# Kernel optimization log

Hardware: AMD Instinct MI355X
Metric: run time of the kernel (lower is better)

The kernel has to match this reference:

```python
import jax, jax.numpy as jnp
import numpy as np

B, NPG, FDIM = 128, 32, 128      # graphs, nodes per graph, feature dim
N = B * NPG                       # 4096 total nodes
DEG = 8
E = N * DEG                       # 32768 intra-graph edges
RATIO = 0.5                       # ASAPooling ratio
ALPHA = 0.2                       # GCN2Conv alpha
EPS = 1e-5                        # InstanceNorm eps
SLOPE = 0.2                       # ASAPooling leaky_relu slope


def _w(k, shape, fan_in):
    return jax.random.normal(k, shape, dtype=jnp.float32) / np.float32(np.sqrt(fan_in))


def setup_inputs():
    key = jax.random.key(0)
    ks = jax.random.split(key, 40)
    x = jax.random.normal(ks[0], (N, FDIM), dtype=jnp.float32)
    # intra-graph random edges (uniform 32-node graphs)
    eg = jnp.repeat(jnp.arange(B, dtype=jnp.int32), E // B)
    src = eg * NPG + jax.random.randint(ks[1], (E,), 0, NPG, dtype=jnp.int32)
    dst = eg * NPG + jax.random.randint(ks[2], (E,), 0, NPG, dtype=jnp.int32)
    d = {"x": x}
    i = [3]
    def nw(shape, fan):
        w = _w(ks[i[0]], shape, fan); i[0] += 1; return w
    F = FDIM
    for p in ("p1", "p2"):  # ASAPooling 1 / 2 params
        d[p + "_rel_w"] = nw((F, F), F);  d[p + "_rel_b"] = jnp.zeros((F,), jnp.float32)
        d[p + "_root_w"] = nw((F, F), F)
        d[p + "_lin_w"] = nw((F, F), F);  d[p + "_lin_b"] = jnp.zeros((F,), jnp.float32)
        d[p + "_att_w"] = nw((2 * F,), 2 * F);  d[p + "_att_b"] = jnp.zeros((1,), jnp.float32)
        d[p + "_le1_w"] = nw((F, 1), F);  d[p + "_le1_b"] = jnp.zeros((1,), jnp.float32)
        d[p + "_le2_w"] = nw((F, 1), F)
        d[p + "_le3_w"] = nw((F, 1), F);  d[p + "_le3_b"] = jnp.zeros((1,), jnp.float32)
    d["conv1_w"] = nw((F, F), F)
    d["conv2_w"] = nw((F, F), F)
    d["ga_gate_w"] = nw((F, 1), F);  d["ga_gate_b"] = jnp.zeros((1,), jnp.float32)
    d["ga_nn_w"] = nw((F, F), F);    d["ga_nn_b"] = jnp.zeros((F,), jnp.float32)
    d["edge_index"] = jnp.stack([src, dst])
    d["batch"] = jnp.repeat(jnp.arange(B, dtype=jnp.int32), NPG)
    return d


def _seg_softmax(logits, seg, num):
    m = jax.ops.segment_max(logits, seg, num)
    e = jnp.exp(logits - m[seg])
    return e / jax.ops.segment_sum(e, seg, num)[seg]


def _leaky(v):
    return jnp.where(v > 0, v, SLOPE * v)


def _inst_norm(h, seg, num):
    cnt = jax.ops.segment_sum(jnp.ones((h.shape[0],), h.dtype), seg, num)
    mean = jax.ops.segment_sum(h, seg, num) / cnt[:, None]
    hc = h - mean[seg]
    var = jax.ops.segment_sum(hc * hc, seg, num) / cnt[:, None]
    return hc / jnp.sqrt(var + EPS)[seg]


def _gcn2_dense(A, h, x0, W):
    # A: 0/1 adjacency [K,K] with self-loops on diag; gcn_norm then GCN2Conv (beta=1)
    dinv = 1.0 / jnp.sqrt(A.sum(axis=0))
    An = dinv[:, None] * A * dinv[None, :]
    return ((1.0 - ALPHA) * (An.T @ h) + ALPHA * x0) @ W


def _topk_perm(fit, npg, k):
    # per-graph top-k on uniform-size graphs (PyG topk, descending order)
    nb = fit.shape[0] // npg
    idx = jnp.argsort(-fit.reshape(nb, npg), axis=1)[:, :k]
    return (idx + (jnp.arange(nb) * npg)[:, None]).reshape(-1)


def _asap_dense(A, x, rel_w, rel_b, root_w, lin_w, lin_b, att_w, att_b,
                le1_w, le1_b, le2_w, le3_w, le3_b, npg):
    # ASAPooling on a dense 0/1 adjacency (self-loops already on diag, weight 1)
    K, C = x.shape
    mask = A > 0
    x_pool = (A.T @ x) @ rel_w + rel_b + x @ root_w          # GraphConv
    neg = jnp.asarray(-jnp.inf, x.dtype)
    def colmax(col):  # masked max over source rows, one channel at a time
        return jnp.max(jnp.where(mask, col[:, None], neg), axis=0)
    x_q = jax.lax.map(colmax, x_pool.T).T @ lin_w + lin_b
    logits = _leaky((x_pool @ att_w[C:])[:, None] + (x_q @ att_w[:C])[None, :] + att_b[0])
    S = jax.nn.softmax(jnp.where(mask, logits, neg), axis=0)  # softmax over incoming edges
    S = jnp.where(mask, S, 0.0)
    xc = S.T @ x                                              # cluster reps
    deg_in = A.sum(axis=0)
    fit = A.T @ (xc @ le1_w + le1_b) - deg_in[:, None] * (xc @ le2_w) + xc @ le3_w + le3_b
    fit = jax.nn.sigmoid(fit[:, 0])                           # LEConv score
    k = int(np.ceil(RATIO * npg))
    perm = _topk_perm(fit, npg, k)
    Ssel = S[:, perm]
    An = Ssel.T @ (A @ Ssel)                                  # S^T A S
    di = jnp.arange(perm.shape[0])
    An = (An.at[di, di].set(1.0) != 0).astype(x.dtype)        # fill_diag; weights discarded
    return (xc * fit[:, None])[perm], An, perm


def _forward(args, edge_index, batch):
    (x, p1_rel_w, p1_rel_b, p1_root_w, p1_lin_w, p1_lin_b, p1_att_w, p1_att_b,
     p1_le1_w, p1_le1_b, p1_le2_w, p1_le3_w, p1_le3_b,
     p2_rel_w, p2_rel_b, p2_root_w, p2_lin_w, p2_lin_b, p2_att_w, p2_att_b,
     p2_le1_w, p2_le1_b, p2_le2_w, p2_le3_w, p2_le3_b,
     conv1_w, conv2_w, ga_gate_w, ga_gate_b, ga_nn_w, ga_nn_b) = args
    src0, dst0 = edge_index[0], edge_index[1]
    sl = jnp.arange(N, dtype=src0.dtype)
    src = jnp.concatenate([src0, sl])          # add_remaining_self_loops (weight 1)
    dst = jnp.concatenate([dst0, sl])
    # readout1: mean || max over nodes per graph
    cnt = jax.ops.segment_sum(jnp.ones((N,), x.dtype), batch, B)
    r1 = jnp.hstack([jax.ops.segment_sum(x, batch, B) / cnt[:, None],
                     jax.ops.segment_max(x, batch, B)])
    # ---- ASAPooling 1 (edge-list form) ----
    agg = jax.ops.segment_sum(x[src], dst, N)
    x_pool = agg @ p1_rel_w + p1_rel_b + x @ p1_root_w        # GraphConv
    x_pool_j = x_pool[src]
    x_q = jax.ops.segment_max(x_pool_j, dst, N) @ p1_lin_w + p1_lin_b
    logits = _leaky(x_q[dst] @ p1_att_w[:FDIM] + x_pool_j @ p1_att_w[FDIM:] + p1_att_b[0])
    score = _seg_softmax(logits, dst, N)
    xc = jax.ops.segment_sum(score[:, None] * x[src], dst, N)
    a = xc @ p1_le1_w + p1_le1_b
    b2 = xc @ p1_le2_w
    fit = jax.ops.segment_sum(a[src] - b2[dst], dst, N) + xc @ p1_le3_w + p1_le3_b  # LEConv
    fit = jax.nn.sigmoid(fit[:, 0])
    K1 = int(np.ceil(RATIO * NPG))
    perm1 = _topk_perm(fit, NPG, K1)
    h = (xc * fit[:, None])[perm1]
    batch1 = batch[perm1]
    # dense coarsening: S^T A S (edge count is data-dependent -> dense pattern)
    S = jnp.zeros((N, N), x.dtype).at[src, dst].add(score)
    A = jnp.zeros((N, N), x.dtype).at[src, dst].add(1.0)
    Ssel = S[:, perm1]
    A2 = Ssel.T @ (A @ Ssel)
    di = jnp.arange(perm1.shape[0])
    A2 = (A2.at[di, di].set(1.0) != 0).astype(x.dtype)        # weights discarded in forward
    x1 = x[perm1]
    # conv1 + InstanceNorm + ReLU
    h = jax.nn.relu(_inst_norm(_gcn2_dense(A2, h, x1, conv1_w), batch1, B))
    cnt1 = jax.ops.segment_sum(jnp.ones((h.shape[0],), x.dtype), batch1, B)
    r2 = jnp.hstack([jax.ops.segment_sum(h, batch1, B) / cnt1[:, None],
                     jax.ops.segment_max(h, batch1, B)])
    # ---- ASAPooling 2 (dense) ----
    h2, A3, perm2 = _asap_dense(A2, h, p2_rel_w, p2_rel_b, p2_root_w, p2_lin_w, p2_lin_b,
                                p2_att_w, p2_att_b, p2_le1_w, p2_le1_b, p2_le2_w,
                                p2_le3_w, p2_le3_b, K1)
    batch2 = batch1[perm2]
    x2 = x1[perm2]
    h2 = jax.nn.relu(_inst_norm(_gcn2_dense(A3, h2, x2, conv2_w), batch2, B))
    # AttentionalAggregation (gate MLP [H,1], nn MLP [H,H])
    gate = _seg_softmax((h2 @ ga_gate_w + ga_gate_b)[:, 0], batch2, B)
    mol = jax.ops.segment_sum(gate[:, None] * (h2 @ ga_nn_w + ga_nn_b), batch2, B)
    return jnp.hstack([mol, r2, r1])  # [B, 5*FDIM]


def reference(x, p1_rel_w, p1_rel_b, p1_root_w, p1_lin_w, p1_lin_b, p1_att_w, p1_att_b,
              p1_le1_w, p1_le1_b, p1_le2_w, p1_le3_w, p1_le3_b,
              p2_rel_w, p2_rel_b, p2_root_w, p2_lin_w, p2_lin_b, p2_att_w, p2_att_b,
              p2_le1_w, p2_le1_b, p2_le2_w, p2_le3_w, p2_le3_b,
              conv1_w, conv2_w, ga_gate_w, ga_gate_b, ga_nn_w, ga_nn_b,
              edge_index, batch):
    return _forward((x, p1_rel_w, p1_rel_b, p1_root_w, p1_lin_w, p1_lin_b, p1_att_w,
                     p1_att_b, p1_le1_w, p1_le1_b, p1_le2_w, p1_le3_w, p1_le3_b,
                     p2_rel_w, p2_rel_b, p2_root_w, p2_lin_w, p2_lin_b, p2_att_w,
                     p2_att_b, p2_le1_w, p2_le1_b, p2_le2_w, p2_le3_w, p2_le3_b,
                     conv1_w, conv2_w, ga_gate_w, ga_gate_b, ga_nn_w, ga_nn_b),
                    edge_index, batch)
```

## Files before the change

kernel.cpp:

```cpp
#include <hip/hip_runtime.h>
#include <hip/hip_bf16.h>

#define NT   1024
#define FD   128
#define NPGc 32
#define Bc   128
#define K1c  16
#define K2c  8
#define EPSc 1e-5f
#define SLOPEc 0.2f

struct Params {
  const float *x;
  const float *p1_rel_w, *p1_rel_b, *p1_root_w, *p1_lin_w, *p1_lin_b,
              *p1_att_w, *p1_att_b, *p1_le1_w, *p1_le1_b, *p1_le2_w,
              *p1_le3_w, *p1_le3_b;
  const float *p2_rel_w, *p2_rel_b, *p2_root_w, *p2_lin_w, *p2_lin_b,
              *p2_att_w, *p2_att_b, *p2_le1_w, *p2_le1_b, *p2_le2_w,
              *p2_le3_w, *p2_le3_b;
  const float *c1w, *c2w, *ggw, *ggb, *gnw, *gnb;
  const int *ei;
  float *out;
  int etot;
};

template<int ROWS, bool FUSE2>
__device__ __forceinline__ void mm128(const float* __restrict__ A1,
                                      const float* __restrict__ W1,
                                      const float* __restrict__ A2s,
                                      const float* __restrict__ W2,
                                      const float* __restrict__ bias,
                                      float* __restrict__ Out, int tid) {
  constexpr int RPG = (ROWS * FD) / NT;
  const int fo = tid & 127;
  const int rbase = (tid >> 7) * RPG;
  float acc[RPG];
#pragma unroll
  for (int r = 0; r < RPG; ++r) acc[r] = bias ? bias[fo] : 0.f;
  for (int k = 0; k < FD; k += 4) {
    const float w10 = W1[(k + 0) * FD + fo];
    const float w11 = W1[(k + 1) * FD + fo];
    const float w12 = W1[(k + 2) * FD + fo];
    const float w13 = W1[(k + 3) * FD + fo];
    float w20, w21, w22, w23;
    if constexpr (FUSE2) {
      w20 = W2[(k + 0) * FD + fo];
      w21 = W2[(k + 1) * FD + fo];
      w22 = W2[(k + 2) * FD + fo];
      w23 = W2[(k + 3) * FD + fo];
    }
#pragma unroll
    for (int r = 0; r < RPG; ++r) {
      const float4 a1 = *reinterpret_cast<const float4*>(&A1[(rbase + r) * FD + k]);
      float a = acc[r];
      if constexpr (FUSE2) {
        const float4 a2 = *reinterpret_cast<const float4*>(&A2s[(rbase + r) * FD + k]);
        a = fmaf(a1.x, w10, a); a = fmaf(a2.x, w20, a);
        a = fmaf(a1.y, w11, a); a = fmaf(a2.y, w21, a);
        a = fmaf(a1.z, w12, a); a = fmaf(a2.z, w22, a);
        a = fmaf(a1.w, w13, a); a = fmaf(a2.w, w23, a);
      } else {
        a = fmaf(a1.x, w10, a);
        a = fmaf(a1.y, w11, a);
        a = fmaf(a1.z, w12, a);
        a = fmaf(a1.w, w13, a);
      }
      acc[r] = a;
    }
  }
#pragma unroll
  for (int r = 0; r < RPG; ++r) Out[(rbase + r) * FD + fo] = acc[r];
}

template<int ROWS, bool WRITE_R2>
__device__ __forceinline__ void instnorm(float* __restrict__ Hs,
                                         float* __restrict__ meanB,
                                         float* __restrict__ rstdB,
                                         float* __restrict__ outMean,
                                         float* __restrict__ outMax,
                                         int tid) {
  constexpr int RPL = ROWS / 4;
  const int col = tid >> 2, ln = tid & 3;
  if (tid < 512) {
    float s = 0.f;
#pragma unroll
    for (int j = 0; j < RPL; ++j) s += Hs[(ln * RPL + j) * FD + col];
    s += __shfl_xor(s, 1); s += __shfl_xor(s, 2);
    if (ln == 0) meanB[col] = s * (1.f / ROWS);
  }
  __syncthreads();
  if (tid < 512) {
    const float mean = meanB[col];
    float v = 0.f;
#pragma unroll
    for (int j = 0; j < RPL; ++j) {
      float d = Hs[(ln * RPL + j) * FD + col] - mean;
      v += d * d;
    }
    v += __shfl_xor(v, 1); v += __shfl_xor(v, 2);
    if (ln == 0) rstdB[col] = 1.f / sqrtf(v * (1.f / ROWS) + EPSc);
  }
  __syncthreads();
  for (int idx = tid; idx < ROWS * FD; idx += NT) {
    const int c = idx & 127;
    float v = (Hs[idx] - meanB[c]) * rstdB[c];
    Hs[idx] = v > 0.f ? v : 0.f;
  }
  __syncthreads();
  if (WRITE_R2 && tid < 512) {
    float s = 0.f, m = -1e30f;
#pragma unroll
    for (int j = 0; j < RPL; ++j) {
      float v = Hs[(ln * RPL + j) * FD + col];
      s += v; m = fmaxf(m, v);
    }
    s += __shfl_xor(s, 1); s += __shfl_xor(s, 2);
    m = fmaxf(m, __shfl_xor(m, 1)); m = fmaxf(m, __shfl_xor(m, 2));
    if (ln == 0) { outMean[col] = s * (1.f / ROWS); outMax[col] = m; }
  }
}

__global__ __launch_bounds__(NT)
void mol_kernel(Params p) {
  const int g = blockIdx.x;
  const int tid = threadIdx.x;

  __shared__ float sx [NPGc * FD];
  __shared__ float bufA[NPGc * FD];
  __shared__ float xp [NPGc * FD];
  __shared__ float xcb[NPGc * FD];
  __shared__ float Am [NPGc * NPGc];
  __shared__ float Sm [NPGc * NPGc];
  __shared__ float Mm [NPGc * K1c];
  __shared__ float Hh [K1c * FD];
  __shared__ float X1 [K1c * FD];
  __shared__ float A2m[K1c * K1c];
  __shared__ float w1pS[FD], w2pS[FD];
  __shared__ float wcS[2];
  __shared__ float fitS[NPGc];
  __shared__ float degI[NPGc];
  __shared__ float dqS[NPGc], dpS[NPGc];
  __shared__ float sA[NPGc], sB[NPGc], sC[NPGc];
  __shared__ int   selS[NPGc];
  __shared__ float gateS[K2c];

  float* Tb  = bufA;
  float* xc2 = bufA;
  float* T2b = bufA + K1c * FD;
  float* ag2 = xp;
  float* xp2 = xp + K1c * FD;
  float* S2m = xcb;
  float* A3m = xcb + 256;
  float* h2b = xcb + 512;
  float* x2b = xcb + 1536;
  float* meanB = Mm;
  float* rstdB = Mm + 256;
  float* partial = bufA;

  {
    const float4* xs = reinterpret_cast<const float4*>(p.x + (size_t)g * NPGc * FD);
    float4* sd = reinterpret_cast<float4*>(sx);
    for (int i = tid; i < NPGc * FD / 4; i += NT) sd[i] = xs[i];
  }
  for (int i = tid; i < NPGc * NPGc; i += NT) Am[i] = 0.f;
  __syncthreads();

  if (tid < FD) {
    float s = 0.f, m = -1e30f;
    for (int i = 0; i < NPGc; ++i) { float v = sx[i * FD + tid]; s += v; m = fmaxf(m, v); }
    p.out[g * 640 + 384 + tid] = s * (1.f / NPGc);
    p.out[g * 640 + 512 + tid] = m;
  }

  {
    const int r = tid >> 3, sub = tid & 7;
    const float4* aw1 = reinterpret_cast<const float4*>(p.p1_att_w);
    const float4* aw2 = reinterpret_cast<const float4*>(p.p2_att_w);
    const float4* l1 = reinterpret_cast<const float4*>(p.p1_lin_w + r * FD);
    const float4* l2 = reinterpret_cast<const float4*>(p.p2_lin_w + r * FD);
    float s1 = 0.f, s2 = 0.f;
#pragma unroll
    for (int t = 0; t < 4; ++t) {
      const int j = sub * 4 + t;
      float4 a = l1[j], b = aw1[j];
      s1 += a.x * b.x + a.y * b.y + a.z * b.z + a.w * b.w;
      float4 c = l2[j], d = aw2[j];
      s2 += c.x * d.x + c.y * d.y + c.z * d.z + c.w * d.w;
    }
    s1 += __shfl_xor(s1, 1); s1 += __shfl_xor(s1, 2); s1 += __shfl_xor(s1, 4);
    s2 += __shfl_xor(s2, 1); s2 += __shfl_xor(s2, 2); s2 += __shfl_xor(s2, 4);
    if (sub == 0) { w1pS[r] = s1; w2pS[r] = s2; }
  }
  if (tid < 128) {
    const int lane = tid & 63;
    const float* bb = (tid < 64) ? p.p1_lin_b : p.p2_lin_b;
    const float* aw = (tid < 64) ? p.p1_att_w : p.p2_att_w;
    float s = bb[lane] * aw[lane] + bb[lane + 64] * aw[lane + 64];
#pragma unroll
    for (int m2 = 1; m2 < 64; m2 <<= 1) s += __shfl_xor(s, m2);
    if (lane == 0) wcS[tid >> 6] = s;
  }

  for (int e = tid; e < p.etot; e += NT) {
    int s = p.ei[e];
    if ((s >> 5) == g) {
      int d = p.ei[p.etot + e] & 31;
      atomicAdd(&Am[(s & 31) * NPGc + d], 1.f);
    }
  }
  if (tid < NPGc) atomicAdd(&Am[tid * NPGc + tid], 1.f);
  __syncthreads();

  if (tid < NPGc) {
    float s = 0.f;
    for (int i = 0; i < NPGc; ++i) s += Am[i * NPGc + tid];
    degI[tid] = s;
  }
  for (int idx = tid; idx < NPGc * FD; idx += NT) {
    int d = idx >> 7, f = idx & 127;
    float s = 0.f;
    for (int i = 0; i < NPGc; ++i) s += Am[i * NPGc + d] * sx[i * FD + f];
    bufA[idx] = s;
  }
  __syncthreads();

  mm128<NPGc, true>(bufA, p.p1_rel_w, sx, p.p1_root_w, p.p1_rel_b, xp, tid);
  __syncthreads();

  {
    const int d = tid >> 5, lane = tid & 31;
    const int f0 = lane * 4;
    float m0 = -1e30f, m1 = -1e30f, m2v = -1e30f, m3 = -1e30f;
    for (int i = 0; i < NPGc; ++i)
      if (Am[i * NPGc + d] > 0.f) {
        const float4 v = *reinterpret_cast<const float4*>(&xp[i * FD + f0]);
        m0 = fmaxf(m0, v.x); m1 = fmaxf(m1, v.y);
        m2v = fmaxf(m2v, v.z); m3 = fmaxf(m3, v.w);
      }
    float s = m0 * w1pS[f0] + m1 * w1pS[f0 + 1] + m2v * w1pS[f0 + 2] + m3 * w1pS[f0 + 3];
#pragma unroll
    for (int m2 = 1; m2 < 32; m2 <<= 1) s += __shfl_xor(s, m2);
    if (lane == 0) dqS[d] = s + wcS[0];
  }
  {
    const int row = tid >> 5, sub = tid & 31;
    float4 a = reinterpret_cast<const float4*>(xp + row * FD)[sub];
    float4 b = reinterpret_cast<const float4*>(p.p1_att_w + FD)[sub];
    float s = a.x * b.x + a.y * b.y + a.z * b.z + a.w * b.w;
#pragma unroll
    for (int m2 = 1; m2 < 32; m2 <<= 1) s += __shfl_xor(s, m2);
    if (sub == 0) dpS[row] = s;
  }
  __syncthreads();

  {
    const int d = tid >> 5, s2 = tid & 31;
    const float ab = p.p1_att_b[0];
    const float mult = Am[s2 * NPGc + d];
    float l = dqS[d] + dpS[s2] + ab;
    l = (l > 0.f) ? l : SLOPEc * l;
    float m = (mult > 0.f) ? l : -1e30f;
#pragma unroll
    for (int m2 = 1; m2 < 32; m2 <<= 1) m = fmaxf(m, __shfl_xor(m, m2));
    float v = (mult > 0.f) ? mult * expf(l - m) : 0.f;
    float den = v;
#pragma unroll
    for (int m2 = 1; m2 < 32; m2 <<= 1) den += __shfl_xor(den, m2);
    Sm[s2 * NPGc + d] = v / den;
  }
  __syncthreads();

  for (int idx = tid; idx < NPGc * FD; idx += NT) {
    int d = idx >> 7, f = idx & 127;
    float s = 0.f;
    for (int i = 0; i < NPGc; ++i) s += Sm[i * NPGc + d] * sx[i * FD + f];
    xcb[idx] = s;
  }
  __syncthreads();

  {
    const int row = tid >> 5, sub = tid & 31;
    float4 xv = reinterpret_cast<const float4*>(xcb + row * FD)[sub];
    float4 wa = reinterpret_cast<const float4*>(p.p1_le1_w)[sub];
    float4 wb = reinterpret_cast<const float4*>(p.p1_le2_w)[sub];
    float4 wc = reinterpret_cast<const float4*>(p.p1_le3_w)[sub];
    float a = xv.x * wa.x + xv.y * wa.y + xv.z * wa.z + xv.w * wa.w;
    float b = xv.x * wb.x + xv.y * wb.y + xv.z * wb.z + xv.w * wb.w;
    float c = xv.x * wc.x + xv.y * wc.y + xv.z * wc.z + xv.w * wc.w;
#pragma unroll
    for (int m2 = 1; m2 < 32; m2 <<= 1) {
      a += __shfl_xor(a, m2); b += __shfl_xor(b, m2); c += __shfl_xor(c, m2);
    }
    if (sub == 0) { sA[row] = a + p.p1_le1_b[0]; sB[row] = b; sC[row] = c; }
  }
  __syncthreads();
  {
    const int d = tid >> 5, i = tid & 31;
    float s = Am[i * NPGc + d] * sA[i];
#pragma unroll
    for (int m2 = 1; m2 < 32; m2 <<= 1) s += __shfl_xor(s, m2);
    if (i == 0) {
      float fv = s - degI[d] * sB[d] + sC[d] + p.p1_le3_b[0];
      fitS[d] = 1.f / (1.f + expf(-fv));
    }
  }
  __syncthreads();

  if (tid < NPGc) {
    float fi = fitS[tid]; int r = 0;
    for (int j = 0; j < NPGc; ++j) { float fj = fitS[j]; r += (fj > fi) || (fj == fi && j < tid); }
    if (r < K1c) selS[r] = tid;
  }
  __syncthreads();

  for (int idx = tid; idx < K1c * FD; idx += NT) {
    int r = idx >> 7, f = idx & 127;
    int n = selS[r] & 31;
    Hh[idx] = xcb[n * FD + f] * fitS[n];
    X1[idx] = sx[n * FD + f];
  }
  __syncthreads();

  for (int idx = tid; idx < NPGc * K1c; idx += NT) {
    int i = idx >> 4, c = idx & 15;
    float s = 0.f; int sc = selS[c] & 31;
    for (int j = 0; j < NPGc; ++j) s += Am[i * NPGc + j] * Sm[j * NPGc + sc];
    Mm[idx] = s;
  }
  __syncthreads();
  for (int idx = tid; idx < K1c * K1c; idx += NT) {
    int r = idx >> 4, c = idx & 15;
    float s = 0.f; int sr = selS[r] & 31;
    for (int i = 0; i < NPGc; ++i) s += Sm[i * NPGc + sr] * Mm[i * K1c + c];
    A2m[idx] = (r == c || s != 0.f) ? 1.f : 0.f;
  }
  __syncthreads();

  if (tid < K1c) {
    float s = 0.f;
    for (int i = 0; i < K1c; ++i) s += A2m[i * K1c + tid];
    dqS[tid] = 1.f / sqrtf(s);
  }
  __syncthreads();
  for (int idx = tid; idx < K1c * FD; idx += NT) {
    int j = idx >> 7, f = idx & 127;
    float s = 0.f;
    for (int i = 0; i < K1c; ++i) s += dqS[i] * A2m[i * K1c + j] * Hh[i * FD + f];
    Tb[idx] = 0.8f * dqS[j] * s + 0.2f * X1[idx];
  }
  __syncthreads();
  mm128<K1c, false>(Tb, p.c1w, nullptr, nullptr, nullptr, Hh, tid);
  __syncthreads();
  instnorm<K1c, true>(Hh, meanB, rstdB,
                      p.out + g * 640 + 128, p.out + g * 640 + 256, tid);
  __syncthreads();

  for (int idx = tid; idx < K1c * FD; idx += NT) {
    int j = idx >> 7, f = idx & 127;
    float s = 0.f;
    for (int i = 0; i < K1c; ++i) s += A2m[i * K1c + j] * Hh[i * FD + f];
    ag2[idx] = s;
  }
  __syncthreads();
  mm128<K1c, true>(ag2, p.p2_rel_w, Hh, p.p2_root_w, p.p2_rel_b, xp2, tid);
  __syncthreads();

  {
    const int j = tid >> 6, lane = tid & 63;
    const int f0 = lane * 2;
    float m0 = -1e30f, m1 = -1e30f;
    for (int i = 0; i < K1c; ++i)
      if (A2m[i * K1c + j] > 0.f) {
        const float2 v = *reinterpret_cast<const float2*>(&xp2[i * FD + f0]);
        m0 = fmaxf(m0, v.x); m1 = fmaxf(m1, v.y);
      }
    float s = m0 * w2pS[f0] + m1 * w2pS[f0 + 1];
#pragma unroll
    for (int m2 = 1; m2 < 64; m2 <<= 1) s += __shfl_xor(s, m2);
    if (lane == 0) dqS[j] = s + wcS[1];
  }
  {
    const int row = tid >> 6, sub = tid & 63;
    float2 a = reinterpret_cast<const float2*>(xp2 + row * FD)[sub];
    float2 b = reinterpret_cast<const float2*>(p.p2_att_w + FD)[sub];
    float s = a.x * b.x + a.y * b.y;
#pragma unroll
    for (int m2 = 1; m2 < 64; m2 <<= 1) s += __shfl_xor(s, m2);
    if (sub == 0) dpS[row] = s;
  }
  __syncthreads();

  if (tid < K1c * K1c) {
    const int j = tid >> 4, i = tid & 15;
    const float ab = p.p2_att_b[0];
    const float av = A2m[i * K1c + j];
    float l = dpS[i] + dqS[j] + ab;
    l = (l > 0.f) ? l : SLOPEc * l;
    float m = (av > 0.f) ? l : -1e30f;
#pragma unroll
    for (int m2 = 1; m2 < 16; m2 <<= 1) m = fmaxf(m, __shfl_xor(m, m2));
    float v = (av > 0.f) ? expf(l - m) : 0.f;
    float den = v;
#pragma unroll
    for (int m2 = 1; m2 < 16; m2 <<= 1) den += __shfl_xor(den, m2);
    S2m[i * K1c + j] = v / den;
  }
  __syncthreads();
  for (int idx = tid; idx < K1c * FD; idx += NT) {
    int j = idx >> 7, f = idx & 127;
    float s = 0.f;
    for (int i = 0; i < K1c; ++i) s += S2m[i * K1c + j] * Hh[i * FD + f];
    xc2[idx] = s;
  }
  __syncthreads();

  {
    const int row = tid >> 6, sub = tid & 63;
    float2 xv = reinterpret_cast<const float2*>(xc2 + row * FD)[sub];
    float2 wa = reinterpret_cast<const float2*>(p.p2_le1_w)[sub];
    float2 wb = reinterpret_cast<const float2*>(p.p2_le2_w)[sub];
    float2 wc = reinterpret_cast<const float2*>(p.p2_le3_w)[sub];
    float a = xv.x * wa.x + xv.y * wa.y;
    float b = xv.x * wb.x + xv.y * wb.y;
    float c = xv.x * wc.x + xv.y * wc.y;
#pragma unroll
    for (int m2 = 1; m2 < 64; m2 <<= 1) {
      a += __shfl_xor(a, m2); b += __shfl_xor(b, m2); c += __shfl_xor(c, m2);
    }
    if (sub == 0) { sA[row] = a + p.p2_le1_b[0]; sB[row] = b; sC[row] = c; }
  }
  __syncthreads();
  if (tid < K1c * K1c) {
    const int j = tid >> 4, i = tid & 15;
    float av = A2m[i * K1c + j];
    float s = av * sA[i];
    float deg = av;
#pragma unroll
    for (int m2 = 1; m2 < 16; m2 <<= 1) {
      s += __shfl_xor(s, m2); deg += __shfl_xor(deg, m2);
    }
    if (i == 0) {
      float fv = s - deg * sB[j] + sC[j] + p.p2_le3_b[0];
      fitS[j] = 1.f / (1.f + expf(-fv));
    }
  }
  __syncthreads();
  if (tid < K1c) {
    float fi = fitS[tid]; int r = 0;
    for (int j = 0; j < K1c; ++j) { float fj = fitS[j]; r += (fj > fi) || (fj == fi && j < tid); }
    if (r < K2c) selS[r] = tid;
  }
  __syncthreads();
  for (int idx = tid; idx < K2c * FD; idx += NT) {
    int r = idx >> 7, f = idx & 127;
    int n = selS[r] & 15;
    h2b[idx] = xc2[n * FD + f] * fitS[n];
    x2b[idx] = X1[n * FD + f];
  }
  for (int idx = tid; idx < K1c * K2c; idx += NT) {
    int i = idx >> 3, c = idx & 7;
    float s = 0.f; int sc = selS[c] & 15;
    for (int j = 0; j < K1c; ++j) s += A2m[i * K1c + j] * S2m[j * K1c + sc];
    Mm[idx] = s;
  }
  __syncthreads();
  for (int idx = tid; idx < K2c * K2c; idx += NT) {
    int r = idx >> 3, c = idx & 7;
    float s = 0.f; int sr = selS[r] & 15;
    for (int i = 0; i < K1c; ++i) s += S2m[i * K1c + sr] * Mm[i * K2c + c];
    A3m[idx] = (r == c || s != 0.f) ? 1.f : 0.f;
  }
  __syncthreads();

  if (tid < K2c) {
    float s = 0.f;
    for (int i = 0; i < K2c; ++i) s += A3m[i * K2c + tid];
    dqS[tid] = 1.f / sqrtf(s);
  }
  __syncthreads();
  for (int idx = tid; idx < K2c * FD; idx += NT) {
    int j = idx >> 7, f = idx & 127;
    float s = 0.f;
    for (int i = 0; i < K2c; ++i) s += dqS[i] * A3m[i * K2c + j] * h2b[i * FD + f];
    T2b[idx] = 0.8f * dqS[j] * s + 0.2f * x2b[idx];
  }
  __syncthreads();
  mm128<K2c, false>(T2b, p.c2w, nullptr, nullptr, nullptr, h2b, tid);
  __syncthreads();
  instnorm<K2c, false>(h2b, meanB, rstdB, nullptr, nullptr, tid);
  __syncthreads();

  {
    const int row = tid >> 6, sub = tid & 63;
    if (row < K2c) {
      const float2 a = reinterpret_cast<const float2*>(h2b + row * FD)[sub];
      const float2 wv = reinterpret_cast<const float2*>(p.ggw)[sub];
      float s = a.x * wv.x + a.y * wv.y;
#pragma unroll
      for (int m2 = 1; m2 < 64; m2 <<= 1) s += __shfl_xor(s, m2);
      if (sub == 0) gateS[row] = s + p.ggb[0];
    }
  }
  __syncthreads();
  if (tid < K2c) {
    float m = -1e30f;
    for (int i = 0; i < K2c; ++i) m = fmaxf(m, gateS[i]);
    float e = expf(gateS[tid] - m);
    float ssum = 0.f;
    for (int i = 0; i < K2c; ++i) ssum += expf(gateS[i] - m);
    sA[tid] = e / ssum;
  }
  __syncthreads();
  if (tid < FD) {
    float s = 0.f;
    for (int r = 0; r < K2c; ++r) s += sA[r] * h2b[r * FD + tid];
    Mm[tid] = s;
  }
  __syncthreads();
  {
    const int grp = tid >> 7, fo = tid & 127;
    float s = 0.f;
    for (int kk = 0; kk < 16; ++kk) {
      const int k = grp * 16 + kk;
      s = fmaf(Mm[k], p.gnw[k * FD + fo], s);
    }
    partial[grp * FD + fo] = s;
  }
  __syncthreads();
  if (tid < FD) {
    float s = p.gnb[tid];
#pragma unroll
    for (int grp = 0; grp < 8; ++grp) s += partial[grp * FD + tid];
    p.out[g * 640 + tid] = s;
  }
}

extern "C" void kernel_launch(void* const* d_in, const int* in_sizes, int n_in,
                              void* d_out, int out_size, void* d_ws, size_t ws_size,
                              hipStream_t stream) {
  (void)n_in; (void)d_ws; (void)ws_size; (void)out_size;
  Params p;
  p.x         = (const float*)d_in[0];
  p.p1_rel_w  = (const float*)d_in[1];
  p.p1_rel_b  = (const float*)d_in[2];
  p.p1_root_w = (const float*)d_in[3];
  p.p1_lin_w  = (const float*)d_in[4];
  p.p1_lin_b  = (const float*)d_in[5];
  p.p1_att_w  = (const float*)d_in[6];
  p.p1_att_b  = (const float*)d_in[7];
  p.p1_le1_w  = (const float*)d_in[8];
  p.p1_le1_b  = (const float*)d_in[9];
  p.p1_le2_w  = (const float*)d_in[10];
  p.p1_le3_w  = (const float*)d_in[11];
  p.p1_le3_b  = (const float*)d_in[12];
  p.p2_rel_w  = (const float*)d_in[13];
  p.p2_rel_b  = (const float*)d_in[14];
  p.p2_root_w = (const float*)d_in[15];
  p.p2_lin_w  = (const float*)d_in[16];
  p.p2_lin_b  = (const float*)d_in[17];
  p.p2_att_w  = (const float*)d_in[18];
  p.p2_att_b  = (const float*)d_in[19];
  p.p2_le1_w  = (const float*)d_in[20];
  p.p2_le1_b  = (const float*)d_in[21];
  p.p2_le2_w  = (const float*)d_in[22];
  p.p2_le3_w  = (const float*)d_in[23];
  p.p2_le3_b  = (const float*)d_in[24];
  p.c1w       = (const float*)d_in[25];
  p.c2w       = (const float*)d_in[26];
  p.ggw       = (const float*)d_in[27];
  p.ggb       = (const float*)d_in[28];
  p.gnw       = (const float*)d_in[29];
  p.gnb       = (const float*)d_in[30];
  p.ei        = (const int*)d_in[31];
  p.out       = (float*)d_out;
  p.etot      = in_sizes[31] / 2;
  mol_kernel<<<dim3(Bc), dim3(NT), 0, stream>>>(p);
}
```

Before: 69.25 us.

## Vectorize shared-memory aggregations, prefetch weights, and fuse instance-norm passes

After: 74.94 us. +8.2%, slower.

```diff
diff --git a/kernel.cpp b/kernel.cpp
--- a/kernel.cpp
+++ b/kernel.cpp
@@ -37,17 +37,25 @@
   float acc[RPG];
 #pragma unroll
   for (int r = 0; r < RPG; ++r) acc[r] = bias ? bias[fo] : 0.f;
+
+  float c10 = W1[0 * FD + fo], c11 = W1[1 * FD + fo],
+        c12 = W1[2 * FD + fo], c13 = W1[3 * FD + fo];
+  float c20 = 0.f, c21 = 0.f, c22 = 0.f, c23 = 0.f;
+  if constexpr (FUSE2) {
+    c20 = W2[0 * FD + fo]; c21 = W2[1 * FD + fo];
+    c22 = W2[2 * FD + fo]; c23 = W2[3 * FD + fo];
+  }
   for (int k = 0; k < FD; k += 4) {
-    const float w10 = W1[(k + 0) * FD + fo];
-    const float w11 = W1[(k + 1) * FD + fo];
-    const float w12 = W1[(k + 2) * FD + fo];
-    const float w13 = W1[(k + 3) * FD + fo];
-    float w20, w21, w22, w23;
-    if constexpr (FUSE2) {
-      w20 = W2[(k + 0) * FD + fo];
-      w21 = W2[(k + 1) * FD + fo];
-      w22 = W2[(k + 2) * FD + fo];
-      w23 = W2[(k + 3) * FD + fo];
+    const int kn = k + 4;
+    float n10 = 0.f, n11 = 0.f, n12 = 0.f, n13 = 0.f;
+    float n20 = 0.f, n21 = 0.f, n22 = 0.f, n23 = 0.f;
+    if (kn < FD) {
+      n10 = W1[(kn + 0) * FD + fo]; n11 = W1[(kn + 1) * FD + fo];
+      n12 = W1[(kn + 2) * FD + fo]; n13 = W1[(kn + 3) * FD + fo];
+      if constexpr (FUSE2) {
+        n20 = W2[(kn + 0) * FD + fo]; n21 = W2[(kn + 1) * FD + fo];
+        n22 = W2[(kn + 2) * FD + fo]; n23 = W2[(kn + 3) * FD + fo];
+      }
     }
 #pragma unroll
     for (int r = 0; r < RPG; ++r) {
@@ -55,18 +63,18 @@
       float a = acc[r];
       if constexpr (FUSE2) {
         const float4 a2 = *reinterpret_cast<const float4*>(&A2s[(rbase + r) * FD + k]);
-        a = fmaf(a1.x, w10, a); a = fmaf(a2.x, w20, a);
-        a = fmaf(a1.y, w11, a); a = fmaf(a2.y, w21, a);
-        a = fmaf(a1.z, w12, a); a = fmaf(a2.z, w22, a);
-        a = fmaf(a1.w, w13, a); a = fmaf(a2.w, w23, a);
+        a = fmaf(a1.x, c10, a); a = fmaf(a2.x, c20, a);
+        a = fmaf(a1.y, c11, a); a = fmaf(a2.y, c21, a);
+        a = fmaf(a1.z, c12, a); a = fmaf(a2.z, c22, a);
+        a = fmaf(a1.w, c13, a); a = fmaf(a2.w, c23, a);
       } else {
-        a = fmaf(a1.x, w10, a);
-        a = fmaf(a1.y, w11, a);
-        a = fmaf(a1.z, w12, a);
-        a = fmaf(a1.w, w13, a);
+        a = fmaf(a1.x, c10, a); a = fmaf(a1.y, c11, a);
+        a = fmaf(a1.z, c12, a); a = fmaf(a1.w, c13, a);
       }
       acc[r] = a;
     }
+    c10 = n10; c11 = n11; c12 = n12; c13 = n13;
+    if constexpr (FUSE2) { c20 = n20; c21 = n21; c22 = n22; c23 = n23; }
   }
 #pragma unroll
   for (int r = 0; r < RPG; ++r) Out[(rbase + r) * FD + fo] = acc[r];
@@ -82,41 +90,37 @@
   constexpr int RPL = ROWS / 4;
   const int col = tid >> 2, ln = tid & 3;
   if (tid < 512) {
-    float s = 0.f;
-#pragma unroll
-    for (int j = 0; j < RPL; ++j) s += Hs[(ln * RPL + j) * FD + col];
-    s += __shfl_xor(s, 1); s += __shfl_xor(s, 2);
-    if (ln == 0) meanB[col] = s * (1.f / ROWS);
-  }
-  __syncthreads();
-  if (tid < 512) {
-    const float mean = meanB[col];
-    float v = 0.f;
-#pragma unroll
-    for (int j = 0; j < RPL; ++j) {
-      float d = Hs[(ln * RPL + j) * FD + col] - mean;
-      v += d * d;
-    }
-    v += __shfl_xor(v, 1); v += __shfl_xor(v, 2);
-    if (ln == 0) rstdB[col] = 1.f / sqrtf(v * (1.f / ROWS) + EPSc);
-  }
-  __syncthreads();
-  for (int idx = tid; idx < ROWS * FD; idx += NT) {
-    const int c = idx & 127;
-    float v = (Hs[idx] - meanB[c]) * rstdB[c];
-    Hs[idx] = v > 0.f ? v : 0.f;
-  }
-  __syncthreads();
-  if (WRITE_R2 && tid < 512) {
-    float s = 0.f, m = -1e30f;
+    float s = 0.f, q = 0.f;
 #pragma unroll
     for (int j = 0; j < RPL; ++j) {
       float v = Hs[(ln * RPL + j) * FD + col];
-      s += v; m = fmaxf(m, v);
+      s += v; q = fmaf(v, v, q);
     }
     s += __shfl_xor(s, 1); s += __shfl_xor(s, 2);
-    m = fmaxf(m, __shfl_xor(m, 1)); m = fmaxf(m, __shfl_xor(m, 2));
-    if (ln == 0) { outMean[col] = s * (1.f / ROWS); outMax[col] = m; }
+    q += __shfl_xor(q, 1); q += __shfl_xor(q, 2);
+    if (ln == 0) {
+      float mean = s * (1.f / ROWS);
+      meanB[col] = mean;
+      float var = q * (1.f / ROWS) - mean * mean;
+      rstdB[col] = 1.f / sqrtf(var + EPSc);
+    }
+  }
+  __syncthreads();
+  if (tid < 512) {
+    const float mean = meanB[col], rstd = rstdB[col];
+    float s = 0.f, m = -1e30f;
+#pragma unroll
+    for (int j = 0; j < RPL; ++j) {
+      float v = (Hs[(ln * RPL + j) * FD + col] - mean) * rstd;
+      v = v > 0.f ? v : 0.f;
+      Hs[(ln * RPL + j) * FD + col] = v;
+      if (WRITE_R2) { s += v; m = fmaxf(m, v); }
+    }
+    if (WRITE_R2) {
+      s += __shfl_xor(s, 1); s += __shfl_xor(s, 2);
+      m = fmaxf(m, __shfl_xor(m, 1)); m = fmaxf(m, __shfl_xor(m, 2));
+      if (ln == 0) { outMean[col] = s * (1.f / ROWS); outMax[col] = m; }
+    }
   }
 }
 
@@ -125,16 +129,16 @@
   const int g = blockIdx.x;
   const int tid = threadIdx.x;
 
-  __shared__ float sx [NPGc * FD];
-  __shared__ float bufA[NPGc * FD];
-  __shared__ float xp [NPGc * FD];
-  __shared__ float xcb[NPGc * FD];
-  __shared__ float Am [NPGc * NPGc];
-  __shared__ float Sm [NPGc * NPGc];
-  __shared__ float Mm [NPGc * K1c];
-  __shared__ float Hh [K1c * FD];
-  __shared__ float X1 [K1c * FD];
-  __shared__ float A2m[K1c * K1c];
+  __shared__ __attribute__((aligned(16))) float sx [NPGc * FD];
+  __shared__ __attribute__((aligned(16))) float bufA[NPGc * FD];
+  __shared__ __attribute__((aligned(16))) float xp [NPGc * FD];
+  __shared__ __attribute__((aligned(16))) float xcb[NPGc * FD];
+  __shared__ __attribute__((aligned(16))) float Am [NPGc * NPGc];
+  __shared__ __attribute__((aligned(16))) float Sm [NPGc * NPGc];
+  __shared__ __attribute__((aligned(16))) float Mm [NPGc * K1c];
+  __shared__ __attribute__((aligned(16))) float Hh [K1c * FD];
+  __shared__ __attribute__((aligned(16))) float X1 [K1c * FD];
+  __shared__ __attribute__((aligned(16))) float A2m[K1c * K1c];
   __shared__ float w1pS[FD], w2pS[FD];
   __shared__ float wcS[2];
   __shared__ float fitS[NPGc];
@@ -157,6 +161,14 @@
   float* rstdB = Mm + 256;
   float* partial = bufA;
 
+  const float4* sx4  = reinterpret_cast<const float4*>(sx);
+  const float4* xcb4 = reinterpret_cast<const float4*>(xcb);
+  const float4* Hh4  = reinterpret_cast<const float4*>(Hh);
+  const float4* X14  = reinterpret_cast<const float4*>(X1);
+  const float4* h2b4 = reinterpret_cast<const float4*>(h2b);
+  const float4* x2b4 = reinterpret_cast<const float4*>(x2b);
+  const float4* xc24 = reinterpret_cast<const float4*>(xc2);
+
   {
     const float4* xs = reinterpret_cast<const float4*>(p.x + (size_t)g * NPGc * FD);
     float4* sd = reinterpret_cast<float4*>(sx);
@@ -216,11 +228,16 @@
     for (int i = 0; i < NPGc; ++i) s += Am[i * NPGc + tid];
     degI[tid] = s;
   }
-  for (int idx = tid; idx < NPGc * FD; idx += NT) {
-    int d = idx >> 7, f = idx & 127;
-    float s = 0.f;
-    for (int i = 0; i < NPGc; ++i) s += Am[i * NPGc + d] * sx[i * FD + f];
-    bufA[idx] = s;
+  {
+    const int d = tid >> 5, f4 = tid & 31;
+    float4 s = {0.f, 0.f, 0.f, 0.f};
+    for (int i = 0; i < NPGc; ++i) {
+      const float a = Am[i * NPGc + d];
+      const float4 v = sx4[i * 32 + f4];
+      s.x = fmaf(a, v.x, s.x); s.y = fmaf(a, v.y, s.y);
+      s.z = fmaf(a, v.z, s.z); s.w = fmaf(a, v.w, s.w);
+    }
+    reinterpret_cast<float4*>(bufA)[d * 32 + f4] = s;
   }
   __syncthreads();
 
@@ -270,17 +287,22 @@
   }
   __syncthreads();
 
-  for (int idx = tid; idx < NPGc * FD; idx += NT) {
-    int d = idx >> 7, f = idx & 127;
-    float s = 0.f;
-    for (int i = 0; i < NPGc; ++i) s += Sm[i * NPGc + d] * sx[i * FD + f];
-    xcb[idx] = s;
+  {
+    const int d = tid >> 5, f4 = tid & 31;
+    float4 s = {0.f, 0.f, 0.f, 0.f};
+    for (int i = 0; i < NPGc; ++i) {
+      const float a = Sm[i * NPGc + d];
+      const float4 v = sx4[i * 32 + f4];
+      s.x = fmaf(a, v.x, s.x); s.y = fmaf(a, v.y, s.y);
+      s.z = fmaf(a, v.z, s.z); s.w = fmaf(a, v.w, s.w);
+    }
+    reinterpret_cast<float4*>(xcb)[d * 32 + f4] = s;
   }
   __syncthreads();
 
   {
     const int row = tid >> 5, sub = tid & 31;
-    float4 xv = reinterpret_cast<const float4*>(xcb + row * FD)[sub];
+    float4 xv = xcb4[row * 32 + sub];
     float4 wa = reinterpret_cast<const float4*>(p.p1_le1_w)[sub];
     float4 wb = reinterpret_cast<const float4*>(p.p1_le2_w)[sub];
     float4 wc = reinterpret_cast<const float4*>(p.p1_le3_w)[sub];
@@ -313,11 +335,14 @@
   }
   __syncthreads();
 
-  for (int idx = tid; idx < K1c * FD; idx += NT) {
-    int r = idx >> 7, f = idx & 127;
-    int n = selS[r] & 31;
-    Hh[idx] = xcb[n * FD + f] * fitS[n];
-    X1[idx] = sx[n * FD + f];
+  if (tid < 512) {
+    const int r = tid >> 5, f4 = tid & 31;
+    const int n = selS[r] & 31;
+    const float fv = fitS[n];
+    const float4 v = xcb4[n * 32 + f4];
+    float4 h; h.x = v.x * fv; h.y = v.y * fv; h.z = v.z * fv; h.w = v.w * fv;
+    reinterpret_cast<float4*>(Hh)[r * 32 + f4] = h;
+    reinterpret_cast<float4*>(X1)[r * 32 + f4] = sx4[n * 32 + f4];
   }
   __syncthreads();
 
@@ -342,11 +367,21 @@
     dqS[tid] = 1.f / sqrtf(s);
   }
   __syncthreads();
-  for (int idx = tid; idx < K1c * FD; idx += NT) {
-    int j = idx >> 7, f = idx & 127;
-    float s = 0.f;
-    for (int i = 0; i < K1c; ++i) s += dqS[i] * A2m[i * K1c + j] * Hh[i * FD + f];
-    Tb[idx] = 0.8f * dqS[j] * s + 0.2f * X1[idx];
+  if (tid < 512) {
+    const int j = tid >> 5, f4 = tid & 31;
+    float4 s = {0.f, 0.f, 0.f, 0.f};
+    for (int i = 0; i < K1c; ++i) {
+      const float w = dqS[i] * A2m[i * K1c + j];
+      const float4 h = Hh4[i * 32 + f4];
+      s.x = fmaf(w, h.x, s.x); s.y = fmaf(w, h.y, s.y);
+      s.z = fmaf(w, h.z, s.z); s.w = fmaf(w, h.w, s.w);
+    }
+    const float4 x1 = X14[j * 32 + f4];
+    const float dj = 0.8f * dqS[j];
+    float4 o;
+    o.x = dj * s.x + 0.2f * x1.x; o.y = dj * s.y + 0.2f * x1.y;
+    o.z = dj * s.z + 0.2f * x1.z; o.w = dj * s.w + 0.2f * x1.w;
+    reinterpret_cast<float4*>(Tb)[j * 32 + f4] = o;
   }
   __syncthreads();
   mm128<K1c, false>(Tb, p.c1w, nullptr, nullptr, nullptr, Hh, tid);
@@ -355,11 +390,16 @@
                       p.out + g * 640 + 128, p.out + g * 640 + 256, tid);
   __syncthreads();
 
-  for (int idx = tid; idx < K1c * FD; idx += NT) {
-    int j = idx >> 7, f = idx & 127;
-    float s = 0.f;
-    for (int i = 0; i < K1c; ++i) s += A2m[i * K1c + j] * Hh[i * FD + f];
-    ag2[idx] = s;
+  if (tid < 512) {
+    const int j = tid >> 5, f4 = tid & 31;
+    float4 s = {0.f, 0.f, 0.f, 0.f};
+    for (int i = 0; i < K1c; ++i) {
+      const float a = A2m[i * K1c + j];
+      const float4 h = Hh4[i * 32 + f4];
+      s.x = fmaf(a, h.x, s.x); s.y = fmaf(a, h.y, s.y);
+      s.z = fmaf(a, h.z, s.z); s.w = fmaf(a, h.w, s.w);
+    }
+    reinterpret_cast<float4*>(ag2)[j * 32 + f4] = s;
   }
   __syncthreads();
   mm128<K1c, true>(ag2, p.p2_rel_w, Hh, p.p2_root_w, p.p2_rel_b, xp2, tid);
@@ -406,11 +446,16 @@
     S2m[i * K1c + j] = v / den;
   }
   __syncthreads();
-  for (int idx = tid; idx < K1c * FD; idx += NT) {
-    int j = idx >> 7, f = idx & 127;
-    float s = 0.f;
-    for (int i = 0; i < K1c; ++i) s += S2m[i * K1c + j] * Hh[i * FD + f];
-    xc2[idx] = s;
+  if (tid < 512) {
+    const int j = tid >> 5, f4 = tid & 31;
+    float4 s = {0.f, 0.f, 0.f, 0.f};
+    for (int i = 0; i < K1c; ++i) {
+      const float a = S2m[i * K1c + j];
+      const float4 h = Hh4[i * 32 + f4];
+      s.x = fmaf(a, h.x, s.x); s.y = fmaf(a, h.y, s.y);
+      s.z = fmaf(a, h.z, s.z); s.w = fmaf(a, h.w, s.w);
+    }
+    reinterpret_cast<float4*>(xc2)[j * 32 + f4] = s;
   }
   __syncthreads();
 
@@ -451,11 +496,14 @@
     if (r < K2c) selS[r] = tid;
   }
   __syncthreads();
-  for (int idx = tid; idx < K2c * FD; idx += NT) {
-    int r = idx >> 7, f = idx & 127;
-    int n = selS[r] & 15;
-    h2b[idx] = xc2[n * FD + f] * fitS[n];
-    x2b[idx] = X1[n * FD + f];
+  if (tid < 256) {
+    const int r = tid >> 5, f4 = tid & 31;
+    const int n = selS[r] & 15;
+    const float fv = fitS[n];
+    const float4 v = xc24[n * 32 + f4];
+    float4 h; h.x = v.x * fv; h.y = v.y * fv; h.z = v.z * fv; h.w = v.w * fv;
+    reinterpret_cast<float4*>(h2b)[r * 32 + f4] = h;
+    reinterpret_cast<float4*>(x2b)[r * 32 + f4] = X14[n * 32 + f4];
   }
   for (int idx = tid; idx < K1c * K2c; idx += NT) {
     int i = idx >> 3, c = idx & 7;
@@ -478,11 +526,21 @@
     dqS[tid] = 1.f / sqrtf(s);
   }
   __syncthreads();
-  for (int idx = tid; idx < K2c * FD; idx += NT) {
-    int j = idx >> 7, f = idx & 127;
-    float s = 0.f;
-    for (int i = 0; i < K2c; ++i) s += dqS[i] * A3m[i * K2c + j] * h2b[i * FD + f];
-    T2b[idx] = 0.8f * dqS[j] * s + 0.2f * x2b[idx];
+  if (tid < 256) {
+    const int j = tid >> 5, f4 = tid & 31;
+    float4 s = {0.f, 0.f, 0.f, 0.f};
+    for (int i = 0; i < K2c; ++i) {
+      const float w = dqS[i] * A3m[i * K2c + j];
+      const float4 h = h2b4[i * 32 + f4];
+      s.x = fmaf(w, h.x, s.x); s.y = fmaf(w, h.y, s.y);
+      s.z = fmaf(w, h.z, s.z); s.w = fmaf(w, h.w, s.w);
+    }
+    const float4 x2 = x2b4[j * 32 + f4];
+    const float dj = 0.8f * dqS[j];
+    float4 o;
+    o.x = dj * s.x + 0.2f * x2.x; o.y = dj * s.y + 0.2f * x2.y;
+    o.z = dj * s.z + 0.2f * x2.z; o.w = dj * s.w + 0.2f * x2.w;
+    reinterpret_cast<float4*>(T2b)[j * 32 + f4] = o;
   }
   __syncthreads();
   mm128<K2c, false>(T2b, p.c2w, nullptr, nullptr, nullptr, h2b, tid);
@@ -502,18 +560,17 @@
     }
   }
   __syncthreads();
-  if (tid < K2c) {
-    float m = -1e30f;
-    for (int i = 0; i < K2c; ++i) m = fmaxf(m, gateS[i]);
-    float e = expf(gateS[tid] - m);
-    float ssum = 0.f;
-    for (int i = 0; i < K2c; ++i) ssum += expf(gateS[i] - m);
-    sA[tid] = e / ssum;
-  }
-  __syncthreads();
   if (tid < FD) {
+    float m = gateS[0];
+#pragma unroll
+    for (int i = 1; i < K2c; ++i) m = fmaxf(m, gateS[i]);
+    float e[K2c]; float den = 0.f;
+#pragma unroll
+    for (int i = 0; i < K2c; ++i) { e[i] = expf(gateS[i] - m); den += e[i]; }
+    const float inv = 1.f / den;
     float s = 0.f;
-    for (int r = 0; r < K2c; ++r) s += sA[r] * h2b[r * FD + tid];
+#pragma unroll
+    for (int r = 0; r < K2c; ++r) s = fmaf(e[r] * inv, h2b[r * FD + tid], s);
     Mm[tid] = s;
   }
   __syncthreads();
```
